# Optimization experiments

Measured on AMD Instinct MI355X. Metric: run time of the kernel, lower is better.

The kernel has to match this reference:

```python
import jax, jax.numpy as jnp
import numpy as np

B, T, D = 2, 2048, 2048
H, HKV, HD = 32, 8, 64
THETA = 3.0
EPS = 1e-6
SCALE = HD ** -0.5


def _rms(x, w):
    # x: [..., HD]
    return x * jax.lax.rsqrt(jnp.mean(x * x, axis=-1, keepdims=True) + EPS) * w


def _rope(x):
    # x: [B, h, T, HD]; interleaved-pair rotation, matching RotaryEmbedding
    hd = x.shape[-1]
    inv_freq = 1.0 / (THETA ** (jnp.arange(0, hd, 2, dtype=jnp.float32) / hd))  # [hd/2]
    t = jnp.arange(x.shape[-2], dtype=jnp.float32)
    f = t[:, None] * inv_freq[None, :]  # [T, hd/2]
    c, s = jnp.cos(f), jnp.sin(f)
    x1, x2 = x[..., 0::2], x[..., 1::2]
    return jnp.stack([x1 * c - x2 * s, x1 * s + x2 * c], axis=-1).reshape(x.shape)


def setup_inputs() -> dict:
    key = jax.random.key(0)
    ks = jax.random.split(key, 6)
    x = jax.random.normal(ks[0], (B, T, D), dtype=jnp.float32)
    w_scale = 1.0 / np.sqrt(D)
    Wq = jax.random.normal(ks[1], (H * HD, D), dtype=jnp.float32) * w_scale
    Wk = jax.random.normal(ks[2], (HKV * HD, D), dtype=jnp.float32) * w_scale
    Wv = jax.random.normal(ks[3], (HKV * HD, D), dtype=jnp.float32) * w_scale
    Wo = jax.random.normal(ks[4], (D, H * HD), dtype=jnp.float32) * (1.0 / np.sqrt(H * HD))
    q_norm_w = jnp.ones((HD,), dtype=jnp.float32)
    k_norm_w = jnp.ones((HD,), dtype=jnp.float32)
    causal = jnp.tril(jnp.ones((T, T), dtype=bool))
    mask = jnp.where(causal, 0.0, -1e9).astype(jnp.float32)[None, None]  # [1,1,T,T]
    return dict(x=x, Wq=Wq, Wk=Wk, Wv=Wv, Wo=Wo, q_norm_w=q_norm_w, k_norm_w=k_norm_w, mask=mask)


def reference(x, Wq, Wk, Wv, Wo, q_norm_w, k_norm_w, mask):
    b, t, _ = x.shape
    q = (x @ Wq.T).reshape(b, t, H, HD).transpose(0, 2, 1, 3)      # [B,H,T,HD]
    k = (x @ Wk.T).reshape(b, t, HKV, HD).transpose(0, 2, 1, 3)    # [B,HKV,T,HD]
    v = (x @ Wv.T).reshape(b, t, HKV, HD).transpose(0, 2, 1, 3)
    q = _rms(q, q_norm_w)
    k = _rms(k, k_norm_w)
    q = _rope(q)
    k = _rope(k)
    rep = H // HKV
    k = jnp.repeat(k, rep, axis=1)  # GQA expansion -> [B,H,T,HD]
    v = jnp.repeat(v, rep, axis=1)
    scores = jnp.einsum('bhqd,bhkd->bhqk', q, k) * SCALE + mask
    attn = jax.nn.softmax(scores, axis=-1)
    out = jnp.einsum('bhqk,bhkd->bhqd', attn, v)
    out = out.transpose(0, 2, 1, 3).reshape(b, t, H * HD)
    return out @ Wo.T
```

## Files before the change

kernel.cpp:

```cpp
#include <hip/hip_runtime.h>
#include <hip/hip_bf16.h>
#include <stdint.h>

#define B_ 2
#define T_ 2048
#define D_ 2048
#define H_ 32
#define HKV_ 8
#define HD_ 64
#define SCALE_ 0.125f

typedef float floatx4 __attribute__((ext_vector_type(4)));
typedef __bf16 bf16x8 __attribute__((ext_vector_type(8)));
typedef __bf16 bf16x4 __attribute__((ext_vector_type(4)));
typedef short short4v __attribute__((ext_vector_type(4)));

__device__ inline floatx4 mfma16(bf16x8 a, bf16x8 b, floatx4 c) {
  return __builtin_amdgcn_mfma_f32_16x16x32_bf16(a, b, c, 0, 0, 0);
}

__device__ inline floatx4 mfma16k16(bf16x4 a, bf16x4 b, floatx4 c) {
#if __has_builtin(__builtin_amdgcn_mfma_f32_16x16x16_bf16)
  return __builtin_amdgcn_mfma_f32_16x16x16_bf16(a, b, c, 0, 0, 0);
#else
  return __builtin_amdgcn_mfma_f32_16x16x16bf16_1k(
      __builtin_bit_cast(short4v, a), __builtin_bit_cast(short4v, b), c, 0, 0, 0);
#endif
}

__device__ inline uint16_t f2bf(float f) {
  union { float f; uint32_t u; } x; x.f = f;
  uint32_t r = x.u + 0x7fffu + ((x.u >> 16) & 1u);
  return (uint16_t)(r >> 16);
}

__device__ inline uint32_t f2bf_pk(float a, float b) {
#if __has_builtin(__builtin_amdgcn_cvt_pk_bf16_f32)
  auto pk = __builtin_amdgcn_cvt_pk_bf16_f32(a, b);
  return __builtin_bit_cast(uint32_t, pk);
#else
  return (uint32_t)f2bf(a) | ((uint32_t)f2bf(b) << 16);
#endif
}

__device__ inline uint32_t pack_p(float a, float b) {
#if __has_builtin(__builtin_amdgcn_cvt_pk_bf16_f32)
  auto pk = __builtin_amdgcn_cvt_pk_bf16_f32(a, b);
  return __builtin_bit_cast(uint32_t, pk);
#else
  return __builtin_amdgcn_perm(__builtin_bit_cast(uint32_t, b),
                               __builtin_bit_cast(uint32_t, a), 0x07060302u);
#endif
}

__device__ inline float fast_exp2(float x) {
#if __has_builtin(__builtin_amdgcn_exp2f)
  return __builtin_amdgcn_exp2f(x);
#else
  return __expf(x * 0.69314718056f);
#endif
}

#if __has_builtin(__builtin_amdgcn_global_load_lds)
#define HAVE_ASYNC_LDS 1
typedef const __attribute__((address_space(1))) uint32_t* gas1_u32;
typedef __attribute__((address_space(3))) uint32_t* las3_u32;
__device__ inline void g2lds16(const uint16_t* g, uint16_t* l) {
  __builtin_amdgcn_global_load_lds((gas1_u32)(const void*)g, (las3_u32)(void*)l, 16, 0, 0);
}
#endif

__global__ __launch_bounds__(256) void cvt_all(
    const float* __restrict__ x, const float* __restrict__ wq,
    const float* __restrict__ wk, const float* __restrict__ wv,
    const float* __restrict__ wo,
    uint16_t* __restrict__ xb, uint16_t* __restrict__ wqb,
    uint16_t* __restrict__ wkb, uint16_t* __restrict__ wvb,
    uint16_t* __restrict__ wob) {
  int i = blockIdx.x * 256 + threadIdx.x;
  const float* src; uint16_t* dst; int off;
  if (i < 2097152)      { src = x;  dst = xb;  off = i; }
  else if (i < 3145728) { src = wq; dst = wqb; off = i - 2097152; }
  else if (i < 3407872) { src = wk; dst = wkb; off = i - 3145728; }
  else if (i < 3670016) { src = wv; dst = wvb; off = i - 3407872; }
  else                  { src = wo; dst = wob; off = i - 3670016; }
  float4 v = ((const float4*)src)[off];
  uint64_t packed = (uint64_t)f2bf_pk(v.x, v.y) | ((uint64_t)f2bf_pk(v.z, v.w) << 32);
  ((uint64_t*)dst)[off] = packed;
}

#define BM 128
#define BN 128
#define BK 64

__device__ inline void stage64(const uint16_t* gbase, uint16_t* lds,
                               int k0, int wave, int lane) {
#ifdef HAVE_ASYNC_LDS
  #pragma unroll
  for (int c = 0; c < 4; c++) {
    int chunk = wave * 4 + c;
    int row = chunk * 8 + (lane >> 3);
    int cg  = (lane & 7) ^ ((lane >> 3) & 7);
    g2lds16(gbase + (size_t)row * D_ + k0 + cg * 8, lds + chunk * 512 + lane * 8);
  }
#else
  #pragma unroll
  for (int c = 0; c < 4; c++) {
    int chunk = wave * 4 + c;
    int row = chunk * 8 + (lane >> 3);
    int cg  = (lane & 7) ^ ((lane >> 3) & 7);
    *(uint4*)&lds[chunk * 512 + lane * 8] =
        *(const uint4*)(gbase + (size_t)row * D_ + k0 + cg * 8);
  }
#endif
}

__device__ inline bf16x8 frag64(const uint16_t* lds, int row, int cg) {
  int pcg = cg ^ (row & 7);
  return *(const bf16x8*)&lds[row * 64 + pcg * 8];
}

#define GEMM_KLOOP(Abase, Bbase)                                          \
  for (int k0 = 0; k0 < D_; k0 += BK) {                                   \
    __syncthreads();                                                      \
    stage64(Abase, As, k0, wave, lane);                                   \
    stage64(Bbase, Bs, k0, wave, lane);                                   \
    __syncthreads();                                                      \
    bf16x8 af[4][2], bfr[4][2];                                           \
    _Pragma("unroll")                                                     \
    for (int i = 0; i < 4; i++) {                                         \
      af[i][0] = frag64(As, wm + i * 16 + r16, quad);                     \
      af[i][1] = frag64(As, wm + i * 16 + r16, 4 + quad);                 \
    }                                                                     \
    _Pragma("unroll")                                                     \
    for (int j = 0; j < 4; j++) {                                         \
      bfr[j][0] = frag64(Bs, wn + j * 16 + r16, quad);                    \
      bfr[j][1] = frag64(Bs, wn + j * 16 + r16, 4 + quad);                \
    }                                                                     \
    _Pragma("unroll")                                                     \
    for (int i = 0; i < 4; i++)                                           \
      _Pragma("unroll")                                                   \
      for (int j = 0; j < 4; j++) {                                       \
        acc[i][j] = mfma16(af[i][0], bfr[j][0], acc[i][j]);               \
        acc[i][j] = mfma16(af[i][1], bfr[j][1], acc[i][j]);               \
      }                                                                   \
  }

__global__ __launch_bounds__(256) void qkv_gemm(
    const uint16_t* __restrict__ Xb, const uint16_t* __restrict__ Wqb,
    const uint16_t* __restrict__ Wkb, const uint16_t* __restrict__ Wvb,
    const float* __restrict__ qnw, const float* __restrict__ knw,
    uint16_t* __restrict__ qbf, uint16_t* __restrict__ kbf,
    uint16_t* __restrict__ vt) {
  __shared__ __align__(16) uint16_t As[BM * BK];
  __shared__ __align__(16) uint16_t Bs[BN * BK];
  const int tid = threadIdx.x;
  const int m0 = blockIdx.y * BM;
  const int n0 = blockIdx.x * BN;

  const uint16_t* Wsrc; int nbase;
  if (n0 < 2048)      { Wsrc = Wqb; nbase = 0; }
  else if (n0 < 2560) { Wsrc = Wkb; nbase = 2048; }
  else                { Wsrc = Wvb; nbase = 2560; }

  const int lane = tid & 63, wave = tid >> 6;
  const int wm = (wave >> 1) * 64, wn = (wave & 1) * 64;
  const int quad = lane >> 4, r16 = lane & 15;
  const uint16_t* Abase = Xb + (size_t)m0 * D_;
  const uint16_t* Bbase = Wsrc + (size_t)(n0 - nbase) * D_;

  floatx4 acc[4][4];
  #pragma unroll
  for (int i = 0; i < 4; i++)
    #pragma unroll
    for (int j = 0; j < 4; j++) acc[i][j] = (floatx4){0.f, 0.f, 0.f, 0.f};

  GEMM_KLOOP(Abase, Bbase)

  if (n0 < 2560) {
    const int isK = (n0 >= 2048);
    const float* nw = isK ? knw : qnw;
    const int head = (n0 - (isK ? 2048 : 0) + wn) >> 6;
    uint16_t* dst = isK ? kbf : qbf;
    const int NH = isK ? HKV_ : H_;
    float wreg[4];
    #pragma unroll
    for (int j = 0; j < 4; j++) wreg[j] = nw[j * 16 + r16];
    float freq[4];
    #pragma unroll
    for (int j = 0; j < 4; j++)
      freq[j] = exp2f((float)(j * 8 + (r16 >> 1)) * -0.0495300781f);
    #pragma unroll
    for (int i = 0; i < 4; i++) {
      #pragma unroll
      for (int r = 0; r < 4; r++) {
        float ss = 0.f;
        #pragma unroll
        for (int j = 0; j < 4; j++) ss += acc[i][j][r] * acc[i][j][r];
        #pragma unroll
        for (int off = 8; off; off >>= 1) ss += __shfl_xor(ss, off);
        float inv = rsqrtf(ss * (1.0f / HD_) + 1e-6f);
        int m = m0 + wm + i * 16 + quad * 4 + r;
        int b = m >> 11, t = m & (T_ - 1);
        size_t rowbase = (((size_t)b * NH + head) * T_ + t) * HD_;
        #pragma unroll
        for (int j = 0; j < 4; j++) {
          float vn = acc[i][j][r] * inv * wreg[j];
          float other = __shfl_xor(vn, 1);
          float f = (float)t * freq[j];
          float s, c;
          __sincosf(f, &s, &c);
          float outv = (r16 & 1) ? (other * s + vn * c) : (vn * c - other * s);
          dst[rowbase + j * 16 + r16] = f2bf(outv);
        }
      }
    }
  } else {
    #pragma unroll
    for (int i = 0; i < 4; i++)
      #pragma unroll
      for (int j = 0; j < 4; j++)
        #pragma unroll
        for (int r = 0; r < 4; r++) {
          int m = m0 + wm + i * 16 + quad * 4 + r;
          int n = n0 + wn + j * 16 + r16 - 2560;
          int b = m >> 11, t = m & (T_ - 1);
          int head = n >> 6, d = n & 63;
          vt[(((size_t)b * HKV_ + head) * HD_ + d) * T_ + t] = f2bf(acc[i][j][r]);
        }
  }
}

__global__ __launch_bounds__(256) void oproj_gemm(
    const uint16_t* __restrict__ Ab, const uint16_t* __restrict__ Bb,
    float* __restrict__ C) {
  __shared__ __align__(16) uint16_t As[BM * BK];
  __shared__ __align__(16) uint16_t Bs[BN * BK];
  const int tid = threadIdx.x;
  const int m0 = blockIdx.y * BM;
  const int n0 = blockIdx.x * BN;
  const int lane = tid & 63, wave = tid >> 6;
  const int wm = (wave >> 1) * 64, wn = (wave & 1) * 64;
  const int quad = lane >> 4, r16 = lane & 15;
  const uint16_t* Abase = Ab + (size_t)m0 * D_;
  const uint16_t* Bbase = Bb + (size_t)n0 * D_;

  floatx4 acc[4][4];
  #pragma unroll
  for (int i = 0; i < 4; i++)
    #pragma unroll
    for (int j = 0; j < 4; j++) acc[i][j] = (floatx4){0.f, 0.f, 0.f, 0.f};

  GEMM_KLOOP(Abase, Bbase)

  #pragma unroll
  for (int i = 0; i < 4; i++)
    #pragma unroll
    for (int j = 0; j < 4; j++)
      #pragma unroll
      for (int r = 0; r < 4; r++) {
        int m = m0 + wm + i * 16 + quad * 4 + r;
        int n = n0 + wn + j * 16 + r16;
        C[(size_t)m * D_ + n] = acc[i][j][r];
      }
}

#define LOG2E 1.44269504089f

__global__ __launch_bounds__(256) void attn(const uint16_t* __restrict__ qb,
                                            const uint16_t* __restrict__ kb,
                                            const uint16_t* __restrict__ vtb,
                                            uint16_t* __restrict__ ao) {
  const int tid = threadIdx.x;
  const int wave = tid >> 6, lane = tid & 63;
  const int quad = lane >> 4, r16 = lane & 15;
  const int h = blockIdx.y, b = blockIdx.z;
  const int kvh = h >> 2;

  const uint16_t* Q  = qb  + ((size_t)b * H_ + h) * T_ * HD_;
  const uint16_t* K  = kb  + ((size_t)b * HKV_ + kvh) * T_ * HD_;
  const uint16_t* Vt = vtb + ((size_t)b * HKV_ + kvh) * (size_t)HD_ * T_;

  __shared__ __align__(16) uint16_t Kl[64 * 64];
  __shared__ __align__(16) uint16_t Vl[64 * 64];

  const int l3 = lane >> 3, l7 = lane & 7, l4 = lane >> 4;
  const int cgK  = l7 ^ l3;
  const int cgV0 = l7 ^ (l4 & 7);
  const int cgV1 = l7 ^ ((4 + l4) & 7);
  uint16_t* KlD0 = Kl + (wave * 16 + 0) * 64 + lane * 8;
  uint16_t* KlD1 = Kl + (wave * 16 + 8) * 64 + lane * 8;
  uint16_t* VlD0 = Vl + (wave * 16 + 0) * 64 + lane * 8;
  uint16_t* VlD1 = Vl + (wave * 16 + 8) * 64 + lane * 8;

  const int koffE0 = r16 * 64 + ((quad)     ^ (r16 & 7)) * 8;
  const int koffE1 = r16 * 64 + ((4 + quad) ^ (r16 & 7)) * 8;
  int voffE[4];
  #pragma unroll
  for (int mt = 0; mt < 4; mt++)
    voffE[mt] = r16 * 64 + (((mt * 2 + (quad >> 1)) ^ ((r16 >> 1) & 7)) * 8) + (quad & 1) * 4;
  float dm[4];
  #pragma unroll
  for (int r = 0; r < 4; r++) dm[r] = (quad * 4 + r <= r16) ? 1.0f : 0.0f;

#define AT_STAGE()                                                        \
  {                                                                       \
    __syncthreads();                                                      \
    g2lds16(kg0, KlD0); g2lds16(kg1, KlD1);                               \
    g2lds16(vg0, VlD0); g2lds16(vg1, VlD1);                               \
    kg0 += 64 * HD_; kg1 += 64 * HD_; vg0 += 64; vg1 += 64;               \
    __syncthreads();                                                      \
  }
#ifndef HAVE_ASYNC_LDS
#undef AT_STAGE
#define AT_STAGE()                                                        \
  {                                                                       \
    uint4 a = *(const uint4*)kg0, bb = *(const uint4*)kg1;                \
    uint4 c = *(const uint4*)vg0, d = *(const uint4*)vg1;                 \
    __syncthreads();                                                      \
    *(uint4*)KlD0 = a; *(uint4*)KlD1 = bb;                                \
    *(uint4*)VlD0 = c; *(uint4*)VlD1 = d;                                 \
    kg0 += 64 * HD_; kg1 += 64 * HD_; vg0 += 64; vg1 += 64;               \
    __syncthreads();                                                      \
  }
#endif

#define AT_CHUNK(mt, MASKED)                                              \
  {                                                                       \
    bf16x8 kf0 = *(const bf16x8*)&Kl[koffE0 + (mt) * 1024];               \
    bf16x8 kf1 = *(const bf16x8*)&Kl[koffE1 + (mt) * 1024];               \
    floatx4 st = (floatx4){0.f, 0.f, 0.f, 0.f};                           \
    st = mfma16(kf0, bq[0], st);                                          \
    st = mfma16(kf1, bq[1], st);                                          \
    float pv[4];                                                          \
    _Pragma("unroll")                                                     \
    for (int r = 0; r < 4; r++) {                                         \
      pv[r] = fast_exp2(fmaf(st[r], SCALE_ * LOG2E, -8.0f * LOG2E));      \
      if (MASKED) pv[r] *= dm[r];                                         \
      l += pv[r];                                                         \
    }                                                                     \
    uint64_t pu = (uint64_t)pack_p(pv[0], pv[1]) |                        \
                  ((uint64_t)pack_p(pv[2], pv[3]) << 32);                 \
    bf16x4 pa = __builtin_bit_cast(bf16x4, pu);                           \
    _Pragma("unroll")                                                     \
    for (int jn = 0; jn < 4; jn++) {                                      \
      bf16x4 vf = *(const bf16x4*)&Vl[voffE[mt] + jn * 1024];             \
      o[jn] = mfma16k16(pa, vf, o[jn]);                                   \
    }                                                                     \
  }

  for (int pass = 0; pass < 2; pass++) {
    const int qt = pass ? (int)blockIdx.x : 31 - (int)blockIdx.x;
    const int q0 = qt * 64;
    const int Rw = q0 + wave * 16;

    bf16x8 bq[2];
    #pragma unroll
    for (int hh = 0; hh < 2; hh++)
      bq[hh] = *(const bf16x8*)(Q + (size_t)(Rw + r16) * HD_ + hh * 32 + quad * 8);

    floatx4 o[4];
    float l = 0.f;
    #pragma unroll
    for (int jn = 0; jn < 4; jn++) o[jn] = (floatx4){0.f, 0.f, 0.f, 0.f};

    const uint16_t* kg0 = K + (size_t)(wave * 16 + l3) * HD_ + cgK * 8;
    const uint16_t* kg1 = K + (size_t)(wave * 16 + 8 + l3) * HD_ + cgK * 8;
    const uint16_t* vg0 = Vt + (size_t)(wave * 16 + l3) * T_ + cgV0 * 8;
    const uint16_t* vg1 = Vt + (size_t)(wave * 16 + 8 + l3) * T_ + cgV1 * 8;

    for (int it = 0; it < qt; it++) {
      AT_STAGE()
      AT_CHUNK(0, false)
      AT_CHUNK(1, false)
      AT_CHUNK(2, false)
      AT_CHUNK(3, false)
    }
    AT_STAGE()
    #pragma unroll
    for (int mt = 0; mt < 4; mt++) {
      if (mt < wave) AT_CHUNK(mt, false)
      else if (mt == wave) AT_CHUNK(mt, true)
    }

    l += __shfl_xor(l, 16);
    l += __shfl_xor(l, 32);
    float lq[4];
    #pragma unroll
    for (int r = 0; r < 4; r++) lq[r] = __shfl(l, quad * 4 + r);

    #pragma unroll
    for (int jn = 0; jn < 4; jn++) {
      uint32_t u01 = f2bf_pk(o[jn][0] / lq[0], o[jn][1] / lq[1]);
      uint32_t u23 = f2bf_pk(o[jn][2] / lq[2], o[jn][3] / lq[3]);
      int t0 = Rw + quad * 4;
      size_t base = ((size_t)b * T_ + t0) * (H_ * HD_) + h * HD_ + jn * 16 + r16;
      ao[base]                = (uint16_t)u01;
      ao[base + 1 * H_ * HD_] = (uint16_t)(u01 >> 16);
      ao[base + 2 * H_ * HD_] = (uint16_t)u23;
      ao[base + 3 * H_ * HD_] = (uint16_t)(u23 >> 16);
    }
  }
#undef AT_STAGE
#undef AT_CHUNK
}

extern "C" void kernel_launch(void* const* d_in, const int* in_sizes, int n_in,
                              void* d_out, int out_size, void* d_ws, size_t ws_size,
                              hipStream_t stream) {
  const float* x  = (const float*)d_in[0];
  const float* Wq = (const float*)d_in[1];
  const float* Wk = (const float*)d_in[2];
  const float* Wv = (const float*)d_in[3];
  const float* Wo = (const float*)d_in[4];
  const float* qw = (const float*)d_in[5];
  const float* kw = (const float*)d_in[6];
  float* out = (float*)d_out;

  char* ws = (char*)d_ws;
  uint16_t* xb  = (uint16_t*)(ws);
  uint16_t* wqb = (uint16_t*)(ws + 16777216);
  uint16_t* wkb = (uint16_t*)(ws + 25165824);
  uint16_t* wvb = (uint16_t*)(ws + 27262976);
  uint16_t* wob = (uint16_t*)(ws + 29360128);
  uint16_t* qbf = (uint16_t*)(ws + 37748736);
  uint16_t* kbf = (uint16_t*)(ws + 54525952);
  uint16_t* vtb = (uint16_t*)(ws + 58720256);
  uint16_t* aob = xb;

  cvt_all<<<18432, 256, 0, stream>>>(x, Wq, Wk, Wv, Wo, xb, wqb, wkb, wvb, wob);

  qkv_gemm<<<dim3(24, 32), 256, 0, stream>>>(xb, wqb, wkb, wvb, qw, kw, qbf, kbf, vtb);

  attn<<<dim3(16, 32, 2), 256, 0, stream>>>(qbf, kbf, vtb, aob);

  oproj_gemm<<<dim3(16, 32), 256, 0, stream>>>(aob, wob, out);
}
```

Baseline: 317.9 us.

## Double-buffer LDS staging in GEMMs and attention to overlap loads with MFMA

Both GEMM kernels now use two LDS buffers with a K-step of 32 instead of a single 64-wide buffer. The next tile is issued into the alternate buffer before computing on the current one, which drops one barrier per iteration. The attention kernel gets the same ping-pong K/V buffers, so the next 64-key tile is loaded while the current one is consumed. The goal is to hide global-to-LDS latency behind MFMA work. In exchange, the GEMM runs twice as many K iterations and barriers with fewer MFMAs between each sync, and the attention kernel uses twice the LDS, which may reduce occupancy.

```diff
diff --git a/kernel.cpp b/kernel.cpp
--- a/kernel.cpp
+++ b/kernel.cpp
@@ -91,59 +91,55 @@
 
 #define BM 128
 #define BN 128
-#define BK 64
-
-__device__ inline void stage64(const uint16_t* gbase, uint16_t* lds,
-                               int k0, int wave, int lane) {
+
+__device__ inline bf16x8 frag32(const uint16_t* lds, int row, int quad) {
+  int pcg = quad ^ ((row >> 1) & 3);
+  return *(const bf16x8*)&lds[row * 32 + pcg * 8];
+}
+
+
+#define GEMM_PROLOGUE()                                                    \
+  const int srow = tid >> 2;                                               \
+  const int scg = (tid & 3) ^ ((tid >> 3) & 3);                            \
+  const uint16_t* gA0 = Abase + (size_t)srow * D_ + scg * 8;               \
+  const uint16_t* gA1 = gA0 + (size_t)64 * D_;                             \
+  const uint16_t* gB0 = Bbase + (size_t)srow * D_ + scg * 8;               \
+  const uint16_t* gB1 = gB0 + (size_t)64 * D_;                             \
+  uint16_t* lA[2] = {As + tid * 8, As + 4096 + tid * 8};                   \
+  uint16_t* lB[2] = {Bs + tid * 8, Bs + 4096 + tid * 8};
+
 #ifdef HAVE_ASYNC_LDS
-  #pragma unroll
-  for (int c = 0; c < 4; c++) {
-    int chunk = wave * 4 + c;
-    int row = chunk * 8 + (lane >> 3);
-    int cg  = (lane & 7) ^ ((lane >> 3) & 7);
-    g2lds16(gbase + (size_t)row * D_ + k0 + cg * 8, lds + chunk * 512 + lane * 8);
-  }
-#else
-  #pragma unroll
-  for (int c = 0; c < 4; c++) {
-    int chunk = wave * 4 + c;
-    int row = chunk * 8 + (lane >> 3);
-    int cg  = (lane & 7) ^ ((lane >> 3) & 7);
-    *(uint4*)&lds[chunk * 512 + lane * 8] =
-        *(const uint4*)(gbase + (size_t)row * D_ + k0 + cg * 8);
-  }
-#endif
-}
-
-__device__ inline bf16x8 frag64(const uint16_t* lds, int row, int cg) {
-  int pcg = cg ^ (row & 7);
-  return *(const bf16x8*)&lds[row * 64 + pcg * 8];
-}
-
-#define GEMM_KLOOP(Abase, Bbase)                                          \
-  for (int k0 = 0; k0 < D_; k0 += BK) {                                   \
-    __syncthreads();                                                      \
-    stage64(Abase, As, k0, wave, lane);                                   \
-    stage64(Bbase, Bs, k0, wave, lane);                                   \
-    __syncthreads();                                                      \
-    bf16x8 af[4][2], bfr[4][2];                                           \
-    _Pragma("unroll")                                                     \
-    for (int i = 0; i < 4; i++) {                                         \
-      af[i][0] = frag64(As, wm + i * 16 + r16, quad);                     \
-      af[i][1] = frag64(As, wm + i * 16 + r16, 4 + quad);                 \
-    }                                                                     \
-    _Pragma("unroll")                                                     \
-    for (int j = 0; j < 4; j++) {                                         \
-      bfr[j][0] = frag64(Bs, wn + j * 16 + r16, quad);                    \
-      bfr[j][1] = frag64(Bs, wn + j * 16 + r16, 4 + quad);                \
-    }                                                                     \
-    _Pragma("unroll")                                                     \
-    for (int i = 0; i < 4; i++)                                           \
-      _Pragma("unroll")                                                   \
-      for (int j = 0; j < 4; j++) {                                       \
-        acc[i][j] = mfma16(af[i][0], bfr[j][0], acc[i][j]);               \
-        acc[i][j] = mfma16(af[i][1], bfr[j][1], acc[i][j]);               \
-      }                                                                   \
+#define GEMM_STAGE(buf, k)                                                 \
+  { g2lds16(gA0 + (k), lA[buf]); g2lds16(gA1 + (k), lA[buf] + 2048);       \
+    g2lds16(gB0 + (k), lB[buf]); g2lds16(gB1 + (k), lB[buf] + 2048); }
+#else
+#define GEMM_STAGE(buf, k)                                                 \
+  { *(uint4*)lA[buf] = *(const uint4*)(gA0 + (k));                         \
+    *(uint4*)(lA[buf] + 2048) = *(const uint4*)(gA1 + (k));                \
+    *(uint4*)lB[buf] = *(const uint4*)(gB0 + (k));                         \
+    *(uint4*)(lB[buf] + 2048) = *(const uint4*)(gB1 + (k)); }
+#endif
+
+#define GEMM_KLOOP()                                                       \
+  GEMM_PROLOGUE()                                                          \
+  GEMM_STAGE(0, 0)                                                         \
+  int cur = 0;                                                             \
+  for (int k0 = 0; k0 < D_; k0 += 32) {                                    \
+    __syncthreads();                                                       \
+    if (k0 + 32 < D_) { GEMM_STAGE(cur ^ 1, k0 + 32) }                     \
+    const uint16_t* Ac = As + cur * 4096;                                  \
+    const uint16_t* Bc = Bs + cur * 4096;                                  \
+    bf16x8 af[4], bfr[4];                                                  \
+    _Pragma("unroll")                                                      \
+    for (int i = 0; i < 4; i++) af[i] = frag32(Ac, wm + i * 16 + r16, quad); \
+    _Pragma("unroll")                                                      \
+    for (int j = 0; j < 4; j++) bfr[j] = frag32(Bc, wn + j * 16 + r16, quad); \
+    _Pragma("unroll")                                                      \
+    for (int i = 0; i < 4; i++)                                            \
+      _Pragma("unroll")                                                    \
+      for (int j = 0; j < 4; j++)                                          \
+        acc[i][j] = mfma16(af[i], bfr[j], acc[i][j]);                      \
+    cur ^= 1;                                                              \
   }
 
 __global__ __launch_bounds__(256) void qkv_gemm(
@@ -152,8 +148,8 @@
     const float* __restrict__ qnw, const float* __restrict__ knw,
     uint16_t* __restrict__ qbf, uint16_t* __restrict__ kbf,
     uint16_t* __restrict__ vt) {
-  __shared__ __align__(16) uint16_t As[BM * BK];
-  __shared__ __align__(16) uint16_t Bs[BN * BK];
+  __shared__ __align__(16) uint16_t As[2 * BM * 32];
+  __shared__ __align__(16) uint16_t Bs[2 * BN * 32];
   const int tid = threadIdx.x;
   const int m0 = blockIdx.y * BM;
   const int n0 = blockIdx.x * BN;
@@ -175,7 +171,7 @@
     #pragma unroll
     for (int j = 0; j < 4; j++) acc[i][j] = (floatx4){0.f, 0.f, 0.f, 0.f};
 
-  GEMM_KLOOP(Abase, Bbase)
+  GEMM_KLOOP()
 
   if (n0 < 2560) {
     const int isK = (n0 >= 2048);
@@ -234,8 +230,8 @@
 __global__ __launch_bounds__(256) void oproj_gemm(
     const uint16_t* __restrict__ Ab, const uint16_t* __restrict__ Bb,
     float* __restrict__ C) {
-  __shared__ __align__(16) uint16_t As[BM * BK];
-  __shared__ __align__(16) uint16_t Bs[BN * BK];
+  __shared__ __align__(16) uint16_t As[2 * BM * 32];
+  __shared__ __align__(16) uint16_t Bs[2 * BN * 32];
   const int tid = threadIdx.x;
   const int m0 = blockIdx.y * BM;
   const int n0 = blockIdx.x * BN;
@@ -251,7 +247,7 @@
     #pragma unroll
     for (int j = 0; j < 4; j++) acc[i][j] = (floatx4){0.f, 0.f, 0.f, 0.f};
 
-  GEMM_KLOOP(Abase, Bbase)
+  GEMM_KLOOP()
 
   #pragma unroll
   for (int i = 0; i < 4; i++)
@@ -281,17 +277,14 @@
   const uint16_t* K  = kb  + ((size_t)b * HKV_ + kvh) * T_ * HD_;
   const uint16_t* Vt = vtb + ((size_t)b * HKV_ + kvh) * (size_t)HD_ * T_;
 
-  __shared__ __align__(16) uint16_t Kl[64 * 64];
-  __shared__ __align__(16) uint16_t Vl[64 * 64];
+  __shared__ __align__(16) uint16_t Kl[2][64 * 64];
+  __shared__ __align__(16) uint16_t Vl[2][64 * 64];
 
   const int l3 = lane >> 3, l7 = lane & 7, l4 = lane >> 4;
   const int cgK  = l7 ^ l3;
   const int cgV0 = l7 ^ (l4 & 7);
   const int cgV1 = l7 ^ ((4 + l4) & 7);
-  uint16_t* KlD0 = Kl + (wave * 16 + 0) * 64 + lane * 8;
-  uint16_t* KlD1 = Kl + (wave * 16 + 8) * 64 + lane * 8;
-  uint16_t* VlD0 = Vl + (wave * 16 + 0) * 64 + lane * 8;
-  uint16_t* VlD1 = Vl + (wave * 16 + 8) * 64 + lane * 8;
+  const int sOff = wave * 16 * 64 + lane * 8;
 
   const int koffE0 = r16 * 64 + ((quad)     ^ (r16 & 7)) * 8;
   const int koffE1 = r16 * 64 + ((4 + quad) ^ (r16 & 7)) * 8;
@@ -303,32 +296,24 @@
   #pragma unroll
   for (int r = 0; r < 4; r++) dm[r] = (quad * 4 + r <= r16) ? 1.0f : 0.0f;
 
-#define AT_STAGE()                                                        \
-  {                                                                       \
-    __syncthreads();                                                      \
-    g2lds16(kg0, KlD0); g2lds16(kg1, KlD1);                               \
-    g2lds16(vg0, VlD0); g2lds16(vg1, VlD1);                               \
-    kg0 += 64 * HD_; kg1 += 64 * HD_; vg0 += 64; vg1 += 64;               \
-    __syncthreads();                                                      \
-  }
-#ifndef HAVE_ASYNC_LDS
-#undef AT_STAGE
-#define AT_STAGE()                                                        \
-  {                                                                       \
-    uint4 a = *(const uint4*)kg0, bb = *(const uint4*)kg1;                \
-    uint4 c = *(const uint4*)vg0, d = *(const uint4*)vg1;                 \
-    __syncthreads();                                                      \
-    *(uint4*)KlD0 = a; *(uint4*)KlD1 = bb;                                \
-    *(uint4*)VlD0 = c; *(uint4*)VlD1 = d;                                 \
-    kg0 += 64 * HD_; kg1 += 64 * HD_; vg0 += 64; vg1 += 64;               \
-    __syncthreads();                                                      \
-  }
+#ifdef HAVE_ASYNC_LDS
+#define AT_STAGE(buf)                                                     \
+  { g2lds16(kg0, &Kl[buf][sOff]); g2lds16(kg1, &Kl[buf][sOff + 512]);     \
+    g2lds16(vg0, &Vl[buf][sOff]); g2lds16(vg1, &Vl[buf][sOff + 512]);     \
+    kg0 += 64 * HD_; kg1 += 64 * HD_; vg0 += 64; vg1 += 64; }
+#else
+#define AT_STAGE(buf)                                                     \
+  { *(uint4*)&Kl[buf][sOff] = *(const uint4*)kg0;                         \
+    *(uint4*)&Kl[buf][sOff + 512] = *(const uint4*)kg1;                   \
+    *(uint4*)&Vl[buf][sOff] = *(const uint4*)vg0;                         \
+    *(uint4*)&Vl[buf][sOff + 512] = *(const uint4*)vg1;                   \
+    kg0 += 64 * HD_; kg1 += 64 * HD_; vg0 += 64; vg1 += 64; }
 #endif
 
 #define AT_CHUNK(mt, MASKED)                                              \
   {                                                                       \
-    bf16x8 kf0 = *(const bf16x8*)&Kl[koffE0 + (mt) * 1024];               \
-    bf16x8 kf1 = *(const bf16x8*)&Kl[koffE1 + (mt) * 1024];               \
+    bf16x8 kf0 = *(const bf16x8*)&Kc[koffE0 + (mt) * 1024];               \
+    bf16x8 kf1 = *(const bf16x8*)&Kc[koffE1 + (mt) * 1024];               \
     floatx4 st = (floatx4){0.f, 0.f, 0.f, 0.f};                           \
     st = mfma16(kf0, bq[0], st);                                          \
     st = mfma16(kf1, bq[1], st);                                          \
@@ -344,7 +329,7 @@
     bf16x4 pa = __builtin_bit_cast(bf16x4, pu);                           \
     _Pragma("unroll")                                                     \
     for (int jn = 0; jn < 4; jn++) {                                      \
-      bf16x4 vf = *(const bf16x4*)&Vl[voffE[mt] + jn * 1024];             \
+      bf16x4 vf = *(const bf16x4*)&Vc[voffE[mt] + jn * 1024];             \
       o[jn] = mfma16k16(pa, vf, o[jn]);                                   \
     }                                                                     \
   }
@@ -369,18 +354,30 @@
     const uint16_t* vg0 = Vt + (size_t)(wave * 16 + l3) * T_ + cgV0 * 8;
     const uint16_t* vg1 = Vt + (size_t)(wave * 16 + 8 + l3) * T_ + cgV1 * 8;
 
+    __syncthreads();
+    AT_STAGE(0)
+    int cur = 0;
+
     for (int it = 0; it < qt; it++) {
-      AT_STAGE()
+      __syncthreads();
+      AT_STAGE(cur ^ 1)
+      const uint16_t* Kc = Kl[cur];
+      const uint16_t* Vc = Vl[cur];
       AT_CHUNK(0, false)
       AT_CHUNK(1, false)
       AT_CHUNK(2, false)
       AT_CHUNK(3, false)
+      cur ^= 1;
     }
-    AT_STAGE()
-    #pragma unroll
-    for (int mt = 0; mt < 4; mt++) {
-      if (mt < wave) AT_CHUNK(mt, false)
-      else if (mt == wave) AT_CHUNK(mt, true)
+    __syncthreads();
+    {
+      const uint16_t* Kc = Kl[cur];
+      const uint16_t* Vc = Vl[cur];
+      #pragma unroll
+      for (int mt = 0; mt < 4; mt++) {
+        if (mt < wave) AT_CHUNK(mt, false)
+        else if (mt == wave) AT_CHUNK(mt, true)
+      }
     }
 
     l += __shfl_xor(l, 16);
```

Result: no change. 315.5 us (-0.7%).
